# Kernel optimization log

Measured on AMD Instinct MI355X. Metric: run time of the kernel, lower is better.

The kernel has to match this reference:

```python
import jax, jax.numpy as jnp
import numpy as np

EPS = 1e-5
GROUPS = 8
HEADS = 8


def setup_inputs() -> dict:
    key = jax.random.key(0)
    k_x, k_qkv, k_out = jax.random.split(key, 3)
    B, C, X, Y, Z = 2, 256, 16, 16, 16
    x = jax.random.normal(k_x, (B, C, X, Y, Z), dtype=jnp.float32)
    norm_w = jnp.ones((C,), dtype=jnp.float32)
    norm_b = jnp.zeros((C,), dtype=jnp.float32)
    # 1x1 Conv3d weights stored as [out_ch, in_ch]
    w_qkv = jax.random.normal(k_qkv, (3 * C, C), dtype=jnp.float32) * (C ** -0.5)
    w_out = jax.random.normal(k_out, (C, C), dtype=jnp.float32) * (C ** -0.5)
    b_out = jnp.zeros((C,), dtype=jnp.float32)
    return {"x": x, "norm_w": norm_w, "norm_b": norm_b,
            "w_qkv": w_qkv, "w_out": w_out, "b_out": b_out}


def group_norm(x, w, b):
    B, C, X, Y, Z = x.shape
    xg = x.reshape(B, GROUPS, C // GROUPS, X, Y, Z)
    mean = xg.mean(axis=(2, 3, 4, 5), keepdims=True)
    var = xg.var(axis=(2, 3, 4, 5), keepdims=True)
    xn = ((xg - mean) * jax.lax.rsqrt(var + EPS)).reshape(B, C, X, Y, Z)
    return xn * w[None, :, None, None, None] + b[None, :, None, None, None]


def reference(x, norm_w, norm_b, w_qkv, w_out, b_out):
    B, C, X, Y, Z = x.shape
    H = HEADS
    D = C // H
    N = X * Y * Z
    scale = D ** -0.5

    xn = group_norm(x, norm_w, norm_b)
    # 1x1 conv QKV projection (bias=False): [B, 3C, X, Y, Z] flattened to tokens
    qkv = jnp.einsum('oc,bcn->bon', w_qkv, xn.reshape(B, C, N))
    q, k, v = jnp.split(qkv, 3, axis=1)            # each [B, C, N]
    q = q.reshape(B, H, D, N)
    k = k.reshape(B, H, D, N)
    v = v.reshape(B, H, D, N)

    scores = jnp.einsum('bhds,bhdt->bhst', q, k) * scale   # [B, H, N, N]
    probs = jax.nn.softmax(scores, axis=-1)
    out = jnp.einsum('bhst,bhdt->bhds', probs, v)          # [B, H, D, N]
    out = out.reshape(B, C, N)

    # 1x1 conv output projection (with bias)
    out = jnp.einsum('oc,bcn->bon', w_out, out) + b_out[None, :, None]
    return out.reshape(B, C, X, Y, Z) + x
```

## Files before the change

kernel.cpp:

```cpp
#include <hip/hip_runtime.h>

#define NB 2
#define NC 256
#define NT 4096
#define NG 8
#define NH 8
#define EPSV 1e-5f
#define SCALE_L2E 0.25503164427f
#define NCHUNK 4
#define CHTOK (NT / NCHUNK)
#define NIT (CHTOK / 32)
#define PO_ELEMS ((size_t)NB * NC * NT)

typedef __attribute__((ext_vector_type(8))) __bf16 bf16x8;
typedef __attribute__((ext_vector_type(8))) unsigned short u16x8;
typedef __attribute__((ext_vector_type(4))) unsigned short u16x4;
typedef __attribute__((ext_vector_type(4))) unsigned int u32x4;
typedef __attribute__((ext_vector_type(2))) unsigned int u32x2;
typedef __attribute__((ext_vector_type(4))) float f32x4;

static __device__ __forceinline__ unsigned short f2bf(float f) {
    union { float f; unsigned int u; } v; v.f = f;
    unsigned int r = v.u + 0x7fffu + ((v.u >> 16) & 1u);
    return (unsigned short)(r >> 16);
}
static __device__ __forceinline__ float bf2f(unsigned short u) {
    union { unsigned int u; float f; } v; v.u = ((unsigned int)u) << 16;
    return v.f;
}
static __device__ __forceinline__ bf16x8 ldbf8(const unsigned short* p) {
    u16x8 u = *(const u16x8*)p;
    return __builtin_bit_cast(bf16x8, u);
}
static __device__ __forceinline__ unsigned int cvtpk(float lo, float hi) {
    unsigned int d;
    asm("v_cvt_pk_bf16_f32 %0, %1, %2" : "=v"(d) : "v"(lo), "v"(hi));
    return d;
}

__global__ __launch_bounds__(256) void k_stats_partial(const float* __restrict__ x,
                                                       float* __restrict__ part) {
    int bg = blockIdx.x >> 5;
    int p  = blockIdx.x & 31;
    const float4* base = (const float4*)(x + (size_t)bg * 131072 + (size_t)p * 4096);
    float s = 0.f, s2 = 0.f;
#pragma unroll
    for (int i = 0; i < 4; ++i) {
        float4 v = base[threadIdx.x + i * 256];
        s  += v.x + v.y + v.z + v.w;
        s2 += v.x * v.x + v.y * v.y + v.z * v.z + v.w * v.w;
    }
    __shared__ float ss[256], sq[256];
    ss[threadIdx.x] = s; sq[threadIdx.x] = s2;
    __syncthreads();
    for (int off = 128; off > 0; off >>= 1) {
        if (threadIdx.x < off) {
            ss[threadIdx.x] += ss[threadIdx.x + off];
            sq[threadIdx.x] += sq[threadIdx.x + off];
        }
        __syncthreads();
    }
    if (threadIdx.x == 0) {
        part[blockIdx.x * 2 + 0] = ss[0];
        part[blockIdx.x * 2 + 1] = sq[0];
    }
}

__global__ __launch_bounds__(64) void k_stats_final(const float* __restrict__ part,
                                                    float* __restrict__ stats) {
    int bg = blockIdx.x;
    float s = 0.f, s2 = 0.f;
    if (threadIdx.x < 32) {
        s  = part[(bg * 32 + threadIdx.x) * 2 + 0];
        s2 = part[(bg * 32 + threadIdx.x) * 2 + 1];
    }
#pragma unroll
    for (int off = 16; off > 0; off >>= 1) {
        s  += __shfl_down(s, off);
        s2 += __shfl_down(s2, off);
    }
    if (threadIdx.x == 0) {
        const float inv = 1.0f / 131072.0f;
        float mean = s * inv;
        float var  = s2 * inv - mean * mean;
        stats[bg * 2 + 0] = mean;
        stats[bg * 2 + 1] = rsqrtf(var + EPSV);
    }
}

__global__ __launch_bounds__(256) void k_wprep(const float* __restrict__ wq,
                                               unsigned short* __restrict__ wq_bf) {
    int idx = (blockIdx.x * 256 + threadIdx.x) * 8;
    float4 a = *(const float4*)(wq + idx);
    float4 c = *(const float4*)(wq + idx + 4);
    u32x4 o = { cvtpk(a.x, a.y), cvtpk(a.z, a.w),
                cvtpk(c.x, c.y), cvtpk(c.z, c.w) };
    *(u32x4*)(wq_bf + idx) = o;
}

__global__ __launch_bounds__(256) void k_xprep(const float* __restrict__ x,
                                               const float* __restrict__ nw,
                                               const float* __restrict__ nbias,
                                               const float* __restrict__ stats,
                                               unsigned short* __restrict__ xnT) {
    __shared__ unsigned short T[64][72];
    int b = blockIdx.z, c0 = blockIdx.y * 64, n0 = blockIdx.x * 64;
    int tid = threadIdx.x;
    int c_l = tid >> 2, nq = (tid & 3) * 16;
    int c = c0 + c_l;
    int grp = c >> 5;
    float mean = stats[(b * NG + grp) * 2 + 0];
    float rstd = stats[(b * NG + grp) * 2 + 1];
    float wsc = nw[c] * rstd;
    float bb  = nbias[c] - mean * wsc;
    const float4* src = (const float4*)(x + ((size_t)(b * NC + c)) * NT + n0 + nq);
#pragma unroll
    for (int i = 0; i < 4; ++i) {
        float4 v = src[i];
        T[nq + i * 4 + 0][c_l] = f2bf(v.x * wsc + bb);
        T[nq + i * 4 + 1][c_l] = f2bf(v.y * wsc + bb);
        T[nq + i * 4 + 2][c_l] = f2bf(v.z * wsc + bb);
        T[nq + i * 4 + 3][c_l] = f2bf(v.w * wsc + bb);
    }
    __syncthreads();
    int n_l = tid >> 2, cq = (tid & 3) * 16;
    unsigned short* dst = xnT + ((size_t)b * NT + n0 + n_l) * 256 + c0 + cq;
    *(u16x8*)dst       = *(const u16x8*)&T[n_l][cq];
    *(u16x8*)(dst + 8) = *(const u16x8*)&T[n_l][cq + 8];
}

__global__ __launch_bounds__(256) void k_qkv_mfma(const unsigned short* __restrict__ wq_bf,
                                                  const unsigned short* __restrict__ xnT,
                                                  unsigned short* __restrict__ qkT,
                                                  unsigned short* __restrict__ vbf) {
    int b = blockIdx.z, o0 = blockIdx.y * 64, n0 = blockIdx.x * 64;
    int tid = threadIdx.x;
    int w = tid >> 6, lane = tid & 63, c16 = lane & 15, g = lane >> 4;
    int n_tok = n0 + w * 16 + c16;
    const unsigned short* Bsrc = xnT + ((size_t)b * NT + n_tok) * 256 + g * 8;
    const unsigned short* Asrc = wq_bf + (size_t)(o0 + c16) * 256 + g * 8;
    f32x4 acc[4] = {};
    for (int kk = 0; kk < 8; ++kk) {
        bf16x8 bfr = ldbf8(Bsrc + kk * 32);
#pragma unroll
        for (int ot = 0; ot < 4; ++ot) {
            bf16x8 afr = ldbf8(Asrc + ot * 16 * 256 + kk * 32);
            acc[ot] = __builtin_amdgcn_mfma_f32_16x16x32_bf16(afr, bfr, acc[ot], 0, 0, 0);
        }
    }
    if (o0 < 512) {
        int qk = o0 >> 8;
        float sc = (qk == 0) ? SCALE_L2E : 1.0f;
#pragma unroll
        for (int ot = 0; ot < 4; ++ot) {
            int ob = o0 + ot * 16 + g * 4;
            int h  = (ob >> 5) & 7;
            int d4 = ob & 31;
            unsigned int u0 = cvtpk(acc[ot][0] * sc, acc[ot][1] * sc);
            unsigned int u1 = cvtpk(acc[ot][2] * sc, acc[ot][3] * sc);
            u16x4 pk = { (unsigned short)(u0 & 0xFFFF), (unsigned short)(u0 >> 16),
                         (unsigned short)(u1 & 0xFFFF), (unsigned short)(u1 >> 16) };
            *(u16x4*)(qkT + ((((size_t)qk * NB + b) * NH + h) * NT + n_tok) * 32 + d4) = pk;
        }
    } else {
#pragma unroll
        for (int ot = 0; ot < 4; ++ot) {
            int ob = (o0 - 512) + ot * 16 + g * 4;
            int h = (ob >> 5) & 7;
            int d = ob & 31;
            unsigned short* dst = vbf + (((size_t)b * NH + h) * 32 + d) * NT + n_tok;
            dst[0]      = f2bf(acc[ot][0]);
            dst[NT]     = f2bf(acc[ot][1]);
            dst[2 * NT] = f2bf(acc[ot][2]);
            dst[3 * NT] = f2bf(acc[ot][3]);
        }
    }
}

__global__ __launch_bounds__(256) void k_attn(const unsigned short* __restrict__ qkT,
                                              const unsigned short* __restrict__ vbf,
                                              unsigned short* __restrict__ pO,
                                              float* __restrict__ pl) {
    __shared__ unsigned short KV[2048];
    __shared__ unsigned int Pd[4][640];
    int bid = blockIdx.x;
    int xcd  = bid & 7;
    int slot = bid >> 3;
    int combo = xcd * 8 + (slot >> 5);
    int sb    = slot & 31;
    int b  = combo >> 5;
    int ch = (combo >> 3) & 3;
    int h  = combo & 7;

    int tid = threadIdx.x;
    int w = tid >> 6, lane = tid & 63, col = lane & 15, g = lane >> 4;
    int s0 = sb * 128 + w * 32;

    const unsigned short* qB = qkT + ((((size_t)0 * NB + b) * NH + h) * NT) * 32;
    const unsigned short* kB = qkT + ((((size_t)1 * NB + b) * NH + h) * NT) * 32;
    const unsigned short* vB = vbf + (((size_t)b * NH + h) * 32) * NT;

    bf16x8 qf[2];
    qf[0] = ldbf8(qB + (size_t)(s0 + col) * 32 + g * 8);
    qf[1] = ldbf8(qB + (size_t)(s0 + 16 + col) * 32 + g * 8);

    u16x8 ou;
#pragma unroll
    for (int j = 0; j < 8; ++j) ou[j] = 0x3F80;
    const bf16x8 ones = __builtin_bit_cast(bf16x8, ou);

    const unsigned short* gs;
    int gstep;
    if (tid < 128) {
        gs = kB + ((size_t)ch * CHTOK) * 32 + tid * 8;
        gstep = 1024;
    } else {
        int idx = tid - 128;
        int d = idx >> 2, tq = (idx & 3) * 8;
        gs = vB + (size_t)d * NT + ch * CHTOK + tq;
        gstep = 32;
    }

    f32x4 oacc[2][2] = {};
    f32x4 lacc[2] = {};
    unsigned int* Pw = Pd[w];

    u16x8 stg = *(const u16x8*)gs;

    for (int it = 0; it < NIT; ++it) {
        __syncthreads();
        *(u16x8*)&KV[tid * 8] = stg;
        __syncthreads();
        if (it + 1 < NIT)
            stg = *(const u16x8*)(gs + (size_t)(it + 1) * gstep);
        bf16x8 k0 = ldbf8(&KV[0] + col * 32 + g * 8);
        bf16x8 k1 = ldbf8(&KV[0] + (16 + col) * 32 + g * 8);
        bf16x8 v0 = ldbf8(&KV[0] + 1024 + col * 32 + g * 8);
        bf16x8 v1 = ldbf8(&KV[0] + 1024 + (16 + col) * 32 + g * 8);
        const f32x4 z = {0.f, 0.f, 0.f, 0.f};
#pragma unroll
        for (int st = 0; st < 2; ++st) {
            int s_l = st * 16 + col;
            f32x4 sa = __builtin_amdgcn_mfma_f32_16x16x32_bf16(k0, qf[st], z, 0, 0, 0);
            f32x4 sb2 = __builtin_amdgcn_mfma_f32_16x16x32_bf16(k1, qf[st], z, 0, 0, 0);
            unsigned int W0 = cvtpk(__builtin_amdgcn_exp2f(sa[0]),
                                    __builtin_amdgcn_exp2f(sa[1]));
            unsigned int W1 = cvtpk(__builtin_amdgcn_exp2f(sa[2]),
                                    __builtin_amdgcn_exp2f(sa[3]));
            unsigned int W2 = cvtpk(__builtin_amdgcn_exp2f(sb2[0]),
                                    __builtin_amdgcn_exp2f(sb2[1]));
            unsigned int W3 = cvtpk(__builtin_amdgcn_exp2f(sb2[2]),
                                    __builtin_amdgcn_exp2f(sb2[3]));
            u32x2 wlo = {W0, W1};
            u32x2 whi = {W2, W3};
            *(u32x2*)&Pw[s_l * 20 + g * 2]     = wlo;
            *(u32x2*)&Pw[s_l * 20 + 8 + g * 2] = whi;
            u32x4 rv = *(const u32x4*)&Pw[s_l * 20 + g * 4];
            bf16x8 pf = __builtin_bit_cast(bf16x8, rv);
            lacc[st]    = __builtin_amdgcn_mfma_f32_16x16x32_bf16(ones, pf, lacc[st], 0, 0, 0);
            oacc[0][st] = __builtin_amdgcn_mfma_f32_16x16x32_bf16(v0, pf, oacc[0][st], 0, 0, 0);
            oacc[1][st] = __builtin_amdgcn_mfma_f32_16x16x32_bf16(v1, pf, oacc[1][st], 0, 0, 0);
        }
    }

    unsigned short* pOc = pO + (size_t)ch * PO_ELEMS;
#pragma unroll
    for (int dt = 0; dt < 2; ++dt)
#pragma unroll
        for (int st = 0; st < 2; ++st) {
            int s = s0 + st * 16 + col;
            unsigned int u0 = cvtpk(oacc[dt][st][0], oacc[dt][st][1]);
            unsigned int u1 = cvtpk(oacc[dt][st][2], oacc[dt][st][3]);
            u16x4 pk = { (unsigned short)(u0 & 0xFFFF), (unsigned short)(u0 >> 16),
                         (unsigned short)(u1 & 0xFFFF), (unsigned short)(u1 >> 16) };
            *(u16x4*)&pOc[((size_t)(b * NT + s)) * 256 + h * 32 + dt * 16 + g * 4] = pk;
        }
    if (g == 0) {
#pragma unroll
        for (int st = 0; st < 2; ++st) {
            int s = s0 + st * 16 + col;
            pl[(((size_t)ch * NB + b) * NH + h) * NT + s] = lacc[st][0];
        }
    }
}

__global__ __launch_bounds__(256) void k_combine(const unsigned short* __restrict__ pO,
                                                 const float* __restrict__ pl,
                                                 unsigned short* __restrict__ attT) {
    int f = blockIdx.x * 256 + threadIdx.x;
    int b  = f >> 18;
    int r  = f & 262143;
    int s  = r >> 6;
    int cq = (r & 63) * 4;
    int h  = cq >> 5;
    float num[4] = {0.f, 0.f, 0.f, 0.f};
    float den = 0.f;
#pragma unroll
    for (int chn = 0; chn < NCHUNK; ++chn) {
        u16x4 ov = *(const u16x4*)&pO[(size_t)chn * PO_ELEMS +
                                      ((size_t)(b * NT + s)) * 256 + cq];
        den += pl[(((size_t)chn * NB + b) * NH + h) * NT + s];
        num[0] += bf2f(ov[0]); num[1] += bf2f(ov[1]);
        num[2] += bf2f(ov[2]); num[3] += bf2f(ov[3]);
    }
    float rd = 1.0f / den;
    u16x4 res = { f2bf(num[0] * rd), f2bf(num[1] * rd),
                  f2bf(num[2] * rd), f2bf(num[3] * rd) };
    *(u16x4*)&attT[((size_t)(b * NT + s)) * 256 + cq] = res;
}

__global__ __launch_bounds__(256) void k_out_mfma(const unsigned short* __restrict__ attT,
                                                  const unsigned short* __restrict__ wo_bf,
                                                  const float* __restrict__ bout,
                                                  const float* __restrict__ x,
                                                  float* __restrict__ out) {
    int b = blockIdx.z, o0 = blockIdx.y * 64, n0 = blockIdx.x * 64;
    int tid = threadIdx.x;
    int w = tid >> 6, lane = tid & 63, c16 = lane & 15, g = lane >> 4;
    int n_tok = n0 + w * 16 + c16;
    const unsigned short* Bsrc = attT + ((size_t)b * NT + n_tok) * 256 + g * 8;
    const unsigned short* Asrc = wo_bf + (size_t)(o0 + c16) * 256 + g * 8;
    f32x4 acc[4] = {};
    for (int kk = 0; kk < 8; ++kk) {
        bf16x8 bfr = ldbf8(Bsrc + kk * 32);
#pragma unroll
        for (int ot = 0; ot < 4; ++ot) {
            bf16x8 afr = ldbf8(Asrc + ot * 16 * 256 + kk * 32);
            acc[ot] = __builtin_amdgcn_mfma_f32_16x16x32_bf16(afr, bfr, acc[ot], 0, 0, 0);
        }
    }
#pragma unroll
    for (int ot = 0; ot < 4; ++ot) {
        int ob = o0 + ot * 16 + g * 4;
#pragma unroll
        for (int rr = 0; rr < 4; ++rr) {
            int o = ob + rr;
            size_t off = ((size_t)(b * NC + o)) * NT + n_tok;
            out[off] = acc[ot][rr] + bout[o] + x[off];
        }
    }
}

extern "C" void kernel_launch(void* const* d_in, const int* in_sizes, int n_in,
                              void* d_out, int out_size, void* d_ws, size_t ws_size,
                              hipStream_t stream) {
    const float* x    = (const float*)d_in[0];
    const float* nw   = (const float*)d_in[1];
    const float* nb   = (const float*)d_in[2];
    const float* wqkv = (const float*)d_in[3];
    const float* wout = (const float*)d_in[4];
    const float* bout = (const float*)d_in[5];
    float* out = (float*)d_out;
    char* wsb = (char*)d_ws;

    unsigned short* qkT = (unsigned short*)wsb;
    unsigned short* vbf = (unsigned short*)(wsb + 8u * 1024 * 1024);
    unsigned short* pO  = (unsigned short*)(wsb + 12u * 1024 * 1024);
    float* pl   = (float*)(wsb + 28u * 1024 * 1024);
    float* part = (float*)(wsb + 29u * 1024 * 1024);
    float* stats = part + 1024;
    unsigned short* wo_bf = (unsigned short*)(wsb + 30u * 1024 * 1024);
    unsigned short* xnT   = pO;
    unsigned short* wq_bf = (unsigned short*)(wsb + 16u * 1024 * 1024);
    unsigned short* attT = qkT;

    k_stats_partial<<<512, 256, 0, stream>>>(x, part);
    k_stats_final<<<16, 64, 0, stream>>>(part, stats);
    k_wprep<<<96, 256, 0, stream>>>(wqkv, wq_bf);
    k_wprep<<<32, 256, 0, stream>>>(wout, wo_bf);
    k_xprep<<<dim3(NT / 64, NC / 64, NB), 256, 0, stream>>>(x, nw, nb, stats, xnT);
    k_qkv_mfma<<<dim3(NT / 64, 12, NB), 256, 0, stream>>>(wq_bf, xnT, qkT, vbf);
    k_attn<<<dim3(NB * NCHUNK * NH * 32), 256, 0, stream>>>(qkT, vbf, pO, pl);
    k_combine<<<2048, 256, 0, stream>>>(pO, pl, attT);
    k_out_mfma<<<dim3(NT / 64, NC / 64, NB), 256, 0, stream>>>(attT, wo_bf, bout, x, out);
}
```

Measured before the change: 128.1 us.

## Fuse split-attention combine into output projection and merge weight-prep launches

The chunk-combine step, which normalises the partial attention outputs by their summed denominators, now runs inside the output-projection kernel. Each 512-thread block combines 32 tokens into a padded LDS tile and then runs the MFMA projection from that tile. This removes the global round trip of the attT intermediate and one kernel launch. The two weight bf16 conversion launches are also merged into one. The cost is fewer, larger blocks (256 in total), which may reduce latency hiding in the projection, plus an added barrier.

Measured after the change: 121.5 us. -5.1%, faster.

```diff
diff --git a/kernel.cpp b/kernel.cpp
--- a/kernel.cpp
+++ b/kernel.cpp
@@ -88,14 +88,22 @@
     }
 }
 
-__global__ __launch_bounds__(256) void k_wprep(const float* __restrict__ wq,
-                                               unsigned short* __restrict__ wq_bf) {
-    int idx = (blockIdx.x * 256 + threadIdx.x) * 8;
-    float4 a = *(const float4*)(wq + idx);
-    float4 c = *(const float4*)(wq + idx + 4);
+__global__ __launch_bounds__(256) void k_wprep2(const float* __restrict__ wq,
+                                                const float* __restrict__ wo,
+                                                unsigned short* __restrict__ wq_bf,
+                                                unsigned short* __restrict__ wo_bf) {
+    int bidx = blockIdx.x;
+    const float* src;
+    unsigned short* dst;
+    int off;
+    if (bidx < 96) { src = wq; dst = wq_bf; off = bidx * 2048; }
+    else           { src = wo; dst = wo_bf; off = (bidx - 96) * 2048; }
+    int idx = off + threadIdx.x * 8;
+    float4 a = *(const float4*)(src + idx);
+    float4 c = *(const float4*)(src + idx + 4);
     u32x4 o = { cvtpk(a.x, a.y), cvtpk(a.z, a.w),
                 cvtpk(c.x, c.y), cvtpk(c.z, c.w) };
-    *(u32x4*)(wq_bf + idx) = o;
+    *(u32x4*)(dst + idx) = o;
 }
 
 __global__ __launch_bounds__(256) void k_xprep(const float* __restrict__ x,
@@ -284,41 +292,45 @@
     }
 }
 
-__global__ __launch_bounds__(256) void k_combine(const unsigned short* __restrict__ pO,
-                                                 const float* __restrict__ pl,
-                                                 unsigned short* __restrict__ attT) {
-    int f = blockIdx.x * 256 + threadIdx.x;
-    int b  = f >> 18;
-    int r  = f & 262143;
-    int s  = r >> 6;
-    int cq = (r & 63) * 4;
-    int h  = cq >> 5;
-    float num[4] = {0.f, 0.f, 0.f, 0.f};
-    float den = 0.f;
-#pragma unroll
-    for (int chn = 0; chn < NCHUNK; ++chn) {
-        u16x4 ov = *(const u16x4*)&pO[(size_t)chn * PO_ELEMS +
-                                      ((size_t)(b * NT + s)) * 256 + cq];
-        den += pl[(((size_t)chn * NB + b) * NH + h) * NT + s];
-        num[0] += bf2f(ov[0]); num[1] += bf2f(ov[1]);
-        num[2] += bf2f(ov[2]); num[3] += bf2f(ov[3]);
-    }
-    float rd = 1.0f / den;
-    u16x4 res = { f2bf(num[0] * rd), f2bf(num[1] * rd),
-                  f2bf(num[2] * rd), f2bf(num[3] * rd) };
-    *(u16x4*)&attT[((size_t)(b * NT + s)) * 256 + cq] = res;
-}
-
-__global__ __launch_bounds__(256) void k_out_mfma(const unsigned short* __restrict__ attT,
-                                                  const unsigned short* __restrict__ wo_bf,
-                                                  const float* __restrict__ bout,
-                                                  const float* __restrict__ x,
-                                                  float* __restrict__ out) {
-    int b = blockIdx.z, o0 = blockIdx.y * 64, n0 = blockIdx.x * 64;
+__global__ __launch_bounds__(512) void k_out_fused(const unsigned short* __restrict__ pO,
+                                                   const float* __restrict__ pl,
+                                                   const unsigned short* __restrict__ wo_bf,
+                                                   const float* __restrict__ bout,
+                                                   const float* __restrict__ x,
+                                                   float* __restrict__ out) {
+    __shared__ unsigned short attL[32 * 264];
+    int b = blockIdx.y, n0 = blockIdx.x * 32;
     int tid = threadIdx.x;
+
+#pragma unroll
+    for (int i = 0; i < 4; ++i) {
+        int q = tid * 4 + i;
+        int tok_l = q >> 6;
+        int cq = (q & 63) * 4;
+        int h = cq >> 5;
+        int s = n0 + tok_l;
+        float num[4] = {0.f, 0.f, 0.f, 0.f};
+        float den = 0.f;
+#pragma unroll
+        for (int chn = 0; chn < NCHUNK; ++chn) {
+            u16x4 ov = *(const u16x4*)&pO[(size_t)chn * PO_ELEMS +
+                                          ((size_t)(b * NT + s)) * 256 + cq];
+            den += pl[(((size_t)chn * NB + b) * NH + h) * NT + s];
+            num[0] += bf2f(ov[0]); num[1] += bf2f(ov[1]);
+            num[2] += bf2f(ov[2]); num[3] += bf2f(ov[3]);
+        }
+        float rd = 1.0f / den;
+        u16x4 res = { f2bf(num[0] * rd), f2bf(num[1] * rd),
+                      f2bf(num[2] * rd), f2bf(num[3] * rd) };
+        *(u16x4*)&attL[tok_l * 264 + cq] = res;
+    }
+    __syncthreads();
+
     int w = tid >> 6, lane = tid & 63, c16 = lane & 15, g = lane >> 4;
-    int n_tok = n0 + w * 16 + c16;
-    const unsigned short* Bsrc = attT + ((size_t)b * NT + n_tok) * 256 + g * 8;
+    int tg = w & 1, og = w >> 1;
+    int n_tok = n0 + tg * 16 + c16;
+    int o0 = og * 64;
+    const unsigned short* Bsrc = &attL[(tg * 16 + c16) * 264 + g * 8];
     const unsigned short* Asrc = wo_bf + (size_t)(o0 + c16) * 256 + g * 8;
     f32x4 acc[4] = {};
     for (int kk = 0; kk < 8; ++kk) {
@@ -362,15 +374,12 @@
     unsigned short* wo_bf = (unsigned short*)(wsb + 30u * 1024 * 1024);
     unsigned short* xnT   = pO;
     unsigned short* wq_bf = (unsigned short*)(wsb + 16u * 1024 * 1024);
-    unsigned short* attT = qkT;
 
     k_stats_partial<<<512, 256, 0, stream>>>(x, part);
     k_stats_final<<<16, 64, 0, stream>>>(part, stats);
-    k_wprep<<<96, 256, 0, stream>>>(wqkv, wq_bf);
-    k_wprep<<<32, 256, 0, stream>>>(wout, wo_bf);
+    k_wprep2<<<128, 256, 0, stream>>>(wqkv, wout, wq_bf, wo_bf);
     k_xprep<<<dim3(NT / 64, NC / 64, NB), 256, 0, stream>>>(x, nw, nb, stats, xnT);
     k_qkv_mfma<<<dim3(NT / 64, 12, NB), 256, 0, stream>>>(wq_bf, xnT, qkT, vbf);
     k_attn<<<dim3(NB * NCHUNK * NH * 32), 256, 0, stream>>>(qkT, vbf, pO, pl);
-    k_combine<<<2048, 256, 0, stream>>>(pO, pl, attT);
-    k_out_mfma<<<dim3(NT / 64, NC / 64, NB), 256, 0, stream>>>(attT, wo_bf, bout, x, out);
-}
+    k_out_fused<<<dim3(128, NB), 512, 0, stream>>>(pO, pl, wo_bf, bout, x, out);
+}
```
